# Optimization experiments

Measured on AMD Instinct MI355X. Metric: run time of the kernel, lower is better.

## Reference

```python
import jax, jax.numpy as jnp
import numpy as np
from jax import lax

B = 1024       # number of subgraphs (unique batch ids)
L = 64         # max_seq_len
CIN = 512
COUT = 512
K = 3
SEG = 48       # nodes per subgraph (uniform, <= L)
N = B * SEG
EPS = 1e-5


def setup_inputs() -> dict:
    key = jax.random.key(0)
    k1, k2 = jax.random.split(key, 2)
    x = jax.random.normal(k1, (N, CIN), jnp.float32)
    # sorted segment ids, every id 0..B-1 present (as graph_to_nn_batch assumes)
    batch = (jnp.arange(N) // SEG).astype(jnp.int32)
    conv_w = jax.random.normal(k2, (COUT, CIN, K), jnp.float32) * 0.02
    conv_b = jnp.zeros((COUT,), jnp.float32)
    gamma = jnp.ones((COUT,), jnp.float32)
    beta = jnp.zeros((COUT,), jnp.float32)
    return {"x": x, "batch": batch, "conv_w": conv_w, "conv_b": conv_b,
            "gamma": gamma, "beta": beta}


def _gather_pad(x, batch):
    # position of each node within its segment (batch is sorted)
    n = x.shape[0]
    pos = jnp.arange(n) - jnp.searchsorted(batch, batch)  # first-occurrence offset
    keep = pos < L                                        # truncate overflow rows
    pos_c = jnp.minimum(pos, L - 1)
    xm = jnp.where(keep[:, None], x, jnp.zeros((), x.dtype))
    dense = jnp.zeros((B, L, x.shape[1]), x.dtype).at[batch, pos_c].add(xm)
    return dense.transpose(0, 2, 1)  # [B, C, L]


def reference(x, batch, conv_w, conv_b, gamma, beta):
    dense = _gather_pad(x, batch)                              # [B, CIN, L]
    out = lax.conv_general_dilated(
        dense, conv_w, window_strides=(1,), padding=[(1, 1)],
        dimension_numbers=("NCH", "OIH", "NCH"))               # [B, COUT, L]
    out = out + conv_b[None, :, None]
    # BatchNorm (training-mode batch statistics over batch+length per channel)
    mean = out.mean(axis=(0, 2))
    var = out.var(axis=(0, 2))
    out = (out - mean[None, :, None]) * lax.rsqrt(var + EPS)[None, :, None]
    out = out * gamma[None, :, None] + beta[None, :, None]
    out = jax.nn.relu(out)                                     # dropout = identity (eval)
    # nn_batch_to_graph: permute(1,0,2).reshape(C,-1).T -> [B*L, COUT]
    out_x = out.transpose(1, 0, 2).reshape(COUT, -1).T
    batch_out = (jnp.arange(B * L) // L).astype(jnp.int32)
    return out_x, batch_out
```

## Files before the change

kernel.cpp:

```cpp
#include <hip/hip_runtime.h>
#include <hip/hip_bf16.h>

#define NB 1024
#define CIN_ 512
#define COUT_ 512
#define SEG_ 48
#define NROWS (NB * 64)
#define EPS_ 1e-5f

typedef __attribute__((ext_vector_type(8))) short bf8;
typedef __attribute__((ext_vector_type(8))) unsigned short u16x8;
typedef __attribute__((ext_vector_type(4))) float f4;

__device__ __forceinline__ unsigned short f2bf(float f) {
    unsigned int u = __float_as_uint(f);
    u += 0x7fffu + ((u >> 16) & 1u);
    return (unsigned short)(u >> 16);
}

__global__ void prep_x(const float* __restrict__ x, unsigned short* __restrict__ xb) {
    int t = blockIdx.x * 256 + threadIdx.x;
    int p  = t & 63;
    int ks = (t >> 6) & 15;
    int b  = t >> 10;
    u16x8 out[4];
    if (p >= 1 && p <= 48) {
        const f4* src = reinterpret_cast<const f4*>(x + ((size_t)(b * SEG_ + p - 1)) * CIN_ + ks * 32);
        #pragma unroll
        for (int lk = 0; lk < 4; ++lk) {
            f4 f0 = src[lk * 2], f1 = src[lk * 2 + 1];
            out[lk][0] = f2bf(f0.x); out[lk][1] = f2bf(f0.y);
            out[lk][2] = f2bf(f0.z); out[lk][3] = f2bf(f0.w);
            out[lk][4] = f2bf(f1.x); out[lk][5] = f2bf(f1.y);
            out[lk][6] = f2bf(f1.z); out[lk][7] = f2bf(f1.w);
        }
    } else {
        u16x8 z = {0,0,0,0,0,0,0,0};
        #pragma unroll
        for (int lk = 0; lk < 4; ++lk) out[lk] = z;
    }
    #pragma unroll
    for (int lk = 0; lk < 4; ++lk)
        *reinterpret_cast<u16x8*>(xb + (((size_t)(b * 16 + ks) * 4 + lk) * 512 + p * 8)) = out[lk];
}

__global__ void prep_w(const float* __restrict__ w, unsigned short* __restrict__ wtfb) {
    int i = blockIdx.x * 256 + threadIdx.x;
    int c8  = i & 7;
    int cop = (i >> 3) & 255;
    int lk  = (i >> 11) & 3;
    int ks  = (i >> 13) & 15;
    int rest = i >> 17;
    int ch = rest / 3, s = rest % 3;
    int co = ch * 256 + cop;
    int ci = ks * 32 + lk * 8 + c8;
    wtfb[i] = f2bf(w[((size_t)co * CIN_ + ci) * 3 + s]);
}

template<int S, int MT>
__device__ __forceinline__ void phase_mma(const char* Bb, const char* Aseg,
                                          int lr, int lk, int wc, f4 (&acc)[4][4]) {
    const char* Bp = Bb + (((lk << 8) + (wc << 6) + lr) << 4);
    const char* Ap = Aseg + (((lk << 6) + lr + S) << 4);
    bf8 bb[4], af[MT];
    #pragma unroll
    for (int nt = 0; nt < 4; ++nt) bb[nt] = *reinterpret_cast<const bf8*>(Bp + (nt << 8));
    #pragma unroll
    for (int mt = 0; mt < MT; ++mt) af[mt] = *reinterpret_cast<const bf8*>(Ap + (mt << 8));
    __builtin_amdgcn_s_setprio(1);
    #pragma unroll
    for (int mt = 0; mt < MT; ++mt)
        #pragma unroll
        for (int nt = 0; nt < 4; ++nt)
            acc[mt][nt] = __builtin_amdgcn_mfma_f32_16x16x32_bf16(af[mt], bb[nt], acc[mt][nt], 0, 0, 0);
    __builtin_amdgcn_s_setprio(0);
}

#define BARF() { __builtin_amdgcn_sched_barrier(0); __builtin_amdgcn_s_barrier(); __builtin_amdgcn_sched_barrier(0); }
#define WAITV(n) asm volatile("s_waitcnt vmcnt(" #n ")" ::: "memory")

__global__ __launch_bounds__(512, 4) void conv_mfma(
    const unsigned short* __restrict__ xb,
    const unsigned short* __restrict__ wtfb,
    const float* __restrict__ cb,
    float* __restrict__ vout,
    float* __restrict__ psum,
    float* __restrict__ psq)
{
    __shared__ unsigned short sh[32768];
    char* shb = (char*)sh;
    char* Bb0 = shb;
    char* Bb1 = shb + 16384;
    char* Bb2 = shb + 32768;
    char* Aab = shb + 49152;

    const int bid = blockIdx.x;
    const int rb = bid >> 1;
    const int ch = bid & 1;
    const int b2 = rb << 1;
    const int tid = threadIdx.x;
    const int lane = tid & 63;
    const int wv = tid >> 6;
    const int lr = lane & 15;
    const int lk = lane >> 4;
    const int wr = wv >> 2;
    const int wc = wv & 3;

    const char* xc = (const char*)xb;
    const char* wcb = (const char*)wtfb + (size_t)ch * 786432;

    auto stB = [&](const char* chunk, char* dst) {
        const char* s0 = chunk + (wv << 11) + (lane << 4);
        char* d0 = dst + (wv << 11);
        __builtin_amdgcn_global_load_lds((const unsigned int*)s0, (unsigned int*)d0, 16, 0, 0);
        __builtin_amdgcn_global_load_lds((const unsigned int*)(s0 + 1024), (unsigned int*)(d0 + 1024), 16, 0, 0);
    };
    auto chunkA = [&](int b, int ks) { return xc + ((size_t)b * 16 + ks) * 4096; };
    auto chunkB = [&](int s, int ks) { return wcb + (size_t)(s * 16 + ks) * 16384; };
    auto stA = [&](int ksn, char* dst) {
        const char* s0 = ((wv < 4) ? chunkA(b2, ksn) + (wv << 10)
                                   : chunkA(b2 + 1, ksn) + ((wv - 4) << 10)) + (lane << 4);
        __builtin_amdgcn_global_load_lds((const unsigned int*)s0, (unsigned int*)(dst + (wv << 10)), 16, 0, 0);
    };

    f4 acc[4][4];
    #pragma unroll
    for (int mt = 0; mt < 4; ++mt)
        #pragma unroll
        for (int nt = 0; nt < 4; ++nt) { f4 z = {0.f,0.f,0.f,0.f}; acc[mt][nt] = z; }

    stA(0, Aab);
    stB(chunkB(0, 0), Bb0);
    stB(chunkB(1, 0), Bb1);

    #pragma unroll 1
    for (int ks = 0; ks < 16; ++ks) {
        const char* Acur = Aab + ((ks & 1) << 13);
        char* Anxt = (ks < 15) ? (Aab + (((ks + 1) & 1) << 13)) : Bb0;
        const char* Aseg = Acur + (wr << 12);
        const int ksn = (ks < 15) ? ks + 1 : 0;

        stB(chunkB(2, ks), Bb2);
        WAITV(4);
        BARF();
        phase_mma<0, 4>(Bb0, Aseg, lr, lk, wc, acc);
        BARF();

        stB(chunkB(0, ksn), Bb0);
        stA(ksn, Anxt);
        WAITV(5);
        BARF();
        phase_mma<1, 3>(Bb1, Aseg, lr, lk, wc, acc);
        BARF();

        stB(chunkB(1, ksn), Bb1);
        WAITV(5);
        BARF();
        phase_mma<2, 3>(Bb2, Aseg, lr, lk, wc, acc);
        BARF();
    }

    const int co_base = (ch << 8) + (wc << 6);
    const int seg = b2 + wr;
    #pragma unroll
    for (int nt = 0; nt < 4; ++nt) {
        const int co = co_base + (nt << 4) + lr;
        const float bias = cb[co];
        float s1 = 0.f, s2 = 0.f;
        #pragma unroll
        for (int mt = 0; mt < 4; ++mt) {
            #pragma unroll
            for (int r = 0; r < 4; ++r) {
                float v = acc[mt][nt][r] + bias;
                s1 += v; s2 += v * v;
                int l = (mt << 4) + (lk << 2) + r;
                vout[(((size_t)seg << 6) + l) * COUT_ + co] = v;
            }
        }
        s1 += __shfl_xor(s1, 16);
        s1 += __shfl_xor(s1, 32);
        s2 += __shfl_xor(s2, 16);
        s2 += __shfl_xor(s2, 32);
        if (lk == 0) {
            psum[seg * COUT_ + co] = s1;
            psq[seg * COUT_ + co] = s2;
        }
    }
}

__global__ void reduce1(const float* __restrict__ psum, const float* __restrict__ psq,
                        float* __restrict__ t1, float* __restrict__ t2) {
    int co = threadIdx.x;
    int j = blockIdx.x;
    float s1 = 0.f, s2 = 0.f;
    #pragma unroll
    for (int k = 0; k < 8; ++k) {
        int i = j * 8 + k;
        s1 += psum[i * COUT_ + co];
        s2 += psq[i * COUT_ + co];
    }
    t1[j * COUT_ + co] = s1;
    t2[j * COUT_ + co] = s2;
}

__global__ void reduce2(const float* __restrict__ t1, const float* __restrict__ t2,
                        const float* __restrict__ gamma, const float* __restrict__ beta,
                        float* __restrict__ scsh) {
    int co = threadIdx.x;
    float s1 = 0.f, s2 = 0.f;
    for (int j = 0; j < 128; ++j) {
        s1 += t1[j * COUT_ + co];
        s2 += t2[j * COUT_ + co];
    }
    float mean = s1 * (1.f / NROWS);
    float var = s2 * (1.f / NROWS) - mean * mean;
    float rstd = rsqrtf(var + EPS_);
    float sc = gamma[co] * rstd;
    scsh[co] = sc;
    scsh[COUT_ + co] = beta[co] - mean * sc;
}

__global__ void bn_relu(float* __restrict__ vout, const float* __restrict__ scsh) {
    const size_t total = (size_t)NROWS * COUT_ / 4;
    for (size_t i = (size_t)blockIdx.x * blockDim.x + threadIdx.x; i < total;
         i += (size_t)gridDim.x * blockDim.x) {
        f4 v = reinterpret_cast<f4*>(vout)[i];
        int co = (int)((i << 2) & (COUT_ - 1));
        f4 sc = *reinterpret_cast<const f4*>(scsh + co);
        f4 sh = *reinterpret_cast<const f4*>(scsh + COUT_ + co);
        v.x = fmaxf(v.x * sc.x + sh.x, 0.f);
        v.y = fmaxf(v.y * sc.y + sh.y, 0.f);
        v.z = fmaxf(v.z * sc.z + sh.z, 0.f);
        v.w = fmaxf(v.w * sc.w + sh.w, 0.f);
        reinterpret_cast<f4*>(vout)[i] = v;
    }
}

__global__ void write_batch(float* __restrict__ o) {
    int i = blockIdx.x * 256 + threadIdx.x;
    if (i < NROWS) o[i] = (float)(i >> 6);
}

extern "C" void kernel_launch(void* const* d_in, const int* in_sizes, int n_in,
                              void* d_out, int out_size, void* d_ws, size_t ws_size,
                              hipStream_t stream) {
    const float* x      = (const float*)d_in[0];
    const float* conv_w = (const float*)d_in[2];
    const float* conv_b = (const float*)d_in[3];
    const float* gamma  = (const float*)d_in[4];
    const float* beta   = (const float*)d_in[5];

    float* out = (float*)d_out;
    float* out_batch = out + (size_t)NROWS * COUT_;

    char* ws = (char*)d_ws;
    unsigned short* xb   = (unsigned short*)ws;
    size_t off = (size_t)NB * 16 * 2048 * 2;
    unsigned short* wtfb = (unsigned short*)(ws + off);
    off += (size_t)786432 * 2;
    float* psum = (float*)(ws + off);  off += (size_t)NB * COUT_ * 4;
    float* psq  = (float*)(ws + off);  off += (size_t)NB * COUT_ * 4;
    float* t1   = (float*)(ws + off);  off += (size_t)128 * COUT_ * 4;
    float* t2   = (float*)(ws + off);  off += (size_t)128 * COUT_ * 4;
    float* scsh = (float*)(ws + off);

    hipLaunchKernelGGL(prep_x, dim3(NB * 16 * 64 / 256), dim3(256), 0, stream, x, xb);
    hipLaunchKernelGGL(prep_w, dim3(786432 / 256), dim3(256), 0, stream, conv_w, wtfb);
    hipLaunchKernelGGL(conv_mfma, dim3(NB), dim3(512), 0, stream, xb, wtfb, conv_b, out, psum, psq);
    hipLaunchKernelGGL(reduce1, dim3(128), dim3(512), 0, stream, psum, psq, t1, t2);
    hipLaunchKernelGGL(reduce2, dim3(1), dim3(512), 0, stream, t1, t2, gamma, beta, scsh);
    hipLaunchKernelGGL(bn_relu, dim3(2048), dim3(256), 0, stream, out, scsh);
    hipLaunchKernelGGL(write_batch, dim3(NROWS / 256), dim3(256), 0, stream, out_batch);
}
```

Baseline: 169.3 us.

## Rotate four B LDS slots to drop barriers and stage conv output in bf16

The conv kernel now uses four rotating 16KB B buffers in LDS instead of three fixed ones. This lets each phase issue its next weight load right after one barrier, cutting the per-phase barrier count roughly in half. Separately, when the workspace is large enough, the pre-BN conv output is written as bf16 to a scratch buffer and a new bn_relu_bf kernel expands it to fp32. That halves the intermediate write and read traffic but rounds the conv values to bf16 before normalization, and the larger LDS footprint may reduce occupancy.

```diff
diff --git a/kernel.cpp b/kernel.cpp
--- a/kernel.cpp
+++ b/kernel.cpp
@@ -79,20 +79,18 @@
 #define BARF() { __builtin_amdgcn_sched_barrier(0); __builtin_amdgcn_s_barrier(); __builtin_amdgcn_sched_barrier(0); }
 #define WAITV(n) asm volatile("s_waitcnt vmcnt(" #n ")" ::: "memory")
 
+template<bool BF16OUT>
 __global__ __launch_bounds__(512, 4) void conv_mfma(
     const unsigned short* __restrict__ xb,
     const unsigned short* __restrict__ wtfb,
     const float* __restrict__ cb,
-    float* __restrict__ vout,
+    void* __restrict__ vout_,
     float* __restrict__ psum,
     float* __restrict__ psq)
 {
-    __shared__ unsigned short sh[32768];
+    __shared__ unsigned short sh[40960];
     char* shb = (char*)sh;
-    char* Bb0 = shb;
-    char* Bb1 = shb + 16384;
-    char* Bb2 = shb + 32768;
-    char* Aab = shb + 49152;
+    char* Aab = shb + 65536;
 
     const int bid = blockIdx.x;
     const int rb = bid >> 1;
@@ -109,6 +107,7 @@
     const char* xc = (const char*)xb;
     const char* wcb = (const char*)wtfb + (size_t)ch * 786432;
 
+    auto Bslot = [&](int s) { return shb + (s << 14); };
     auto stB = [&](const char* chunk, char* dst) {
         const char* s0 = chunk + (wv << 11) + (lane << 4);
         char* d0 = dst + (wv << 11);
@@ -130,35 +129,35 @@
         for (int nt = 0; nt < 4; ++nt) { f4 z = {0.f,0.f,0.f,0.f}; acc[mt][nt] = z; }
 
     stA(0, Aab);
-    stB(chunkB(0, 0), Bb0);
-    stB(chunkB(1, 0), Bb1);
+    stB(chunkB(0, 0), Bslot(0));
+    stB(chunkB(1, 0), Bslot(1));
+    stB(chunkB(2, 0), Bslot(2));
 
     #pragma unroll 1
     for (int ks = 0; ks < 16; ++ks) {
-        const char* Acur = Aab + ((ks & 1) << 13);
-        char* Anxt = (ks < 15) ? (Aab + (((ks + 1) & 1) << 13)) : Bb0;
-        const char* Aseg = Acur + (wr << 12);
         const int ksn = (ks < 15) ? ks + 1 : 0;
-
-        stB(chunkB(2, ks), Bb2);
+        const int sl = (3 * ks) & 3;
+        const char* Aseg = Aab + ((ks & 1) << 13) + (wr << 12);
+        char* Anxt = Aab + ((ksn & 1) << 13);
+
         WAITV(4);
         BARF();
-        phase_mma<0, 4>(Bb0, Aseg, lr, lk, wc, acc);
+        stB(chunkB(0, ksn), Bslot((sl + 3) & 3));
+        phase_mma<0, 4>(Bslot(sl), Aseg, lr, lk, wc, acc);
+
+        WAITV(4);
         BARF();
-
-        stB(chunkB(0, ksn), Bb0);
         stA(ksn, Anxt);
+        stB(chunkB(1, ksn), Bslot(sl));
+        phase_mma<1, 3>(Bslot((sl + 1) & 3), Aseg, lr, lk, wc, acc);
+
         WAITV(5);
         BARF();
-        phase_mma<1, 3>(Bb1, Aseg, lr, lk, wc, acc);
-        BARF();
-
-        stB(chunkB(1, ksn), Bb1);
-        WAITV(5);
-        BARF();
-        phase_mma<2, 3>(Bb2, Aseg, lr, lk, wc, acc);
-        BARF();
-    }
+        stB(chunkB(2, ksn), Bslot((sl + 1) & 3));
+        phase_mma<2, 3>(Bslot((sl + 2) & 3), Aseg, lr, lk, wc, acc);
+    }
+
+    asm volatile("s_waitcnt vmcnt(0)" ::: "memory");
 
     const int co_base = (ch << 8) + (wc << 6);
     const int seg = b2 + wr;
@@ -174,7 +173,9 @@
                 float v = acc[mt][nt][r] + bias;
                 s1 += v; s2 += v * v;
                 int l = (mt << 4) + (lk << 2) + r;
-                vout[(((size_t)seg << 6) + l) * COUT_ + co] = v;
+                size_t oidx = (((size_t)seg << 6) + l) * COUT_ + co;
+                if (BF16OUT) ((unsigned short*)vout_)[oidx] = f2bf(v);
+                else         ((float*)vout_)[oidx] = v;
             }
         }
         s1 += __shfl_xor(s1, 16);
@@ -218,6 +219,33 @@
     float sc = gamma[co] * rstd;
     scsh[co] = sc;
     scsh[COUT_ + co] = beta[co] - mean * sc;
+}
+
+__global__ void bn_relu_bf(const unsigned short* __restrict__ vb,
+                           const float* __restrict__ scsh, float* __restrict__ out) {
+    const size_t total = (size_t)NROWS * COUT_ / 8;
+    for (size_t i = (size_t)blockIdx.x * blockDim.x + threadIdx.x; i < total;
+         i += (size_t)gridDim.x * blockDim.x) {
+        u16x8 v = reinterpret_cast<const u16x8*>(vb)[i];
+        int co = (int)((i << 3) & (COUT_ - 1));
+        f4 sc0 = *reinterpret_cast<const f4*>(scsh + co);
+        f4 sc1 = *reinterpret_cast<const f4*>(scsh + co + 4);
+        f4 sh0 = *reinterpret_cast<const f4*>(scsh + COUT_ + co);
+        f4 sh1 = *reinterpret_cast<const f4*>(scsh + COUT_ + co + 4);
+        f4 o0, o1;
+        #pragma unroll
+        for (int e = 0; e < 4; ++e) {
+            float f = __uint_as_float(((unsigned int)v[e]) << 16);
+            o0[e] = fmaxf(f * sc0[e] + sh0[e], 0.f);
+        }
+        #pragma unroll
+        for (int e = 0; e < 4; ++e) {
+            float f = __uint_as_float(((unsigned int)v[4 + e]) << 16);
+            o1[e] = fmaxf(f * sc1[e] + sh1[e], 0.f);
+        }
+        reinterpret_cast<f4*>(out)[i * 2] = o0;
+        reinterpret_cast<f4*>(out)[i * 2 + 1] = o1;
+    }
 }
 
 __global__ void bn_relu(float* __restrict__ vout, const float* __restrict__ scsh) {
@@ -262,13 +290,25 @@
     float* psq  = (float*)(ws + off);  off += (size_t)NB * COUT_ * 4;
     float* t1   = (float*)(ws + off);  off += (size_t)128 * COUT_ * 4;
     float* t2   = (float*)(ws + off);  off += (size_t)128 * COUT_ * 4;
-    float* scsh = (float*)(ws + off);
+    float* scsh = (float*)(ws + off);  off += 4096;
+    unsigned short* voutb = (unsigned short*)(ws + off);
+    const bool use_bf16 = (ws_size >= off + (size_t)NROWS * COUT_ * 2);
 
     hipLaunchKernelGGL(prep_x, dim3(NB * 16 * 64 / 256), dim3(256), 0, stream, x, xb);
     hipLaunchKernelGGL(prep_w, dim3(786432 / 256), dim3(256), 0, stream, conv_w, wtfb);
-    hipLaunchKernelGGL(conv_mfma, dim3(NB), dim3(512), 0, stream, xb, wtfb, conv_b, out, psum, psq);
+    if (use_bf16) {
+        hipLaunchKernelGGL((conv_mfma<true>), dim3(NB), dim3(512), 0, stream,
+                           xb, wtfb, conv_b, (void*)voutb, psum, psq);
+    } else {
+        hipLaunchKernelGGL((conv_mfma<false>), dim3(NB), dim3(512), 0, stream,
+                           xb, wtfb, conv_b, (void*)out, psum, psq);
+    }
     hipLaunchKernelGGL(reduce1, dim3(128), dim3(512), 0, stream, psum, psq, t1, t2);
     hipLaunchKernelGGL(reduce2, dim3(1), dim3(512), 0, stream, t1, t2, gamma, beta, scsh);
-    hipLaunchKernelGGL(bn_relu, dim3(2048), dim3(256), 0, stream, out, scsh);
+    if (use_bf16) {
+        hipLaunchKernelGGL(bn_relu_bf, dim3(2048), dim3(256), 0, stream, voutb, scsh, out);
+    } else {
+        hipLaunchKernelGGL(bn_relu, dim3(2048), dim3(256), 0, stream, out, scsh);
+    }
     hipLaunchKernelGGL(write_batch, dim3(NROWS / 256), dim3(256), 0, stream, out_batch);
 }
```

New measurement: 168.4 us. No clear change (-0.5%).
